# Kernel optimization log

Hardware: AMD Instinct MI355X
Metric: run time of the kernel (lower is better)

## Reference

```python
import jax, jax.numpy as jnp
import numpy as np

B, C, H, W = 32, 17, 256, 256


def setup_inputs() -> dict:
    key = jax.random.key(0)
    k1, k2 = jax.random.split(key)
    inp = jax.random.normal(k1, (B, C, H, W), dtype=jnp.float32)
    tgt = jax.random.normal(k2, (B, C, H, W), dtype=jnp.float32)
    masks = jnp.zeros((B, C, H, W), dtype=bool)  # unused by forward
    hull = jnp.zeros((B, 1, H, W), dtype=bool)   # unused by forward
    return {"input": inp, "target": tgt, "masks": masks, "hull": hull}


def reference(input, target, masks, hull):
    # m1: per-(batch, channel) mask of positive target pixels
    m1 = target > 0.0                                  # [B,C,H,W] bool
    # m2: per-batch OR over channels, broadcast back to every channel.
    # (replaces the original O(B*C) Python double loop)
    m2 = jnp.any(m1, axis=1, keepdims=True)            # [B,1,H,W] bool
    diff = jnp.abs(input - target)                     # [B,C,H,W]
    f32 = jnp.float32
    # masked means without data-dependent shapes: sum(mask*diff)/sum(mask)
    mean1 = jnp.sum(jnp.where(m1, diff, f32(0))) / jnp.sum(m1).astype(f32)
    cnt2 = jnp.sum(m2).astype(f32) * f32(diff.shape[1])  # broadcast over C channels
    mean2 = jnp.sum(jnp.where(m2, diff, f32(0))) / cnt2
    return (mean1 + mean2) / f32(2)
```

## Files before the change

kernel.cpp:

```cpp
#include <hip/hip_runtime.h>


#define QPB      16384
#define N_CH     17
#define N_BATCH  32
#define N_QUADS  (N_BATCH * QPB)
#define N_BLOCKS 2048

struct Slot {
    float s1;
    float s2;
    unsigned int c1;
    unsigned int c2;
};

__global__ __launch_bounds__(256) void heatloss_stage1(
    const float* __restrict__ inp, const float* __restrict__ tgt,
    Slot* __restrict__ slots) {

    const int blk = (blockIdx.x & 7) * (N_BLOCKS / 8) + (blockIdx.x >> 3);
    const int q = blk * 256 + threadIdx.x;
    const int b = q >> 14;
    const int r = q & (QPB - 1);

    const float4* __restrict__ tp = (const float4*)tgt + (size_t)b * (N_CH * QPB) + r;
    const float4* __restrict__ xp = (const float4*)inp + (size_t)b * (N_CH * QPB) + r;

    float4 tb[N_CH], xb[N_CH];
    #pragma unroll
    for (int c = 0; c < N_CH; ++c) tb[c] = tp[(size_t)c * QPB];
    #pragma unroll
    for (int c = 0; c < N_CH; ++c) xb[c] = xp[(size_t)c * QPB];

    __builtin_amdgcn_sched_barrier(0);

    float s1 = 0.0f;
    unsigned int c1 = 0u;
    float sa0 = 0.f, sa1 = 0.f, sa2 = 0.f, sa3 = 0.f;
    bool a0 = false, a1 = false, a2 = false, a3 = false;

    #pragma unroll
    for (int c = 0; c < N_CH; ++c) {
        float4 t = tb[c];
        float4 x = xb[c];
        float d0 = fabsf(x.x - t.x);
        float d1 = fabsf(x.y - t.y);
        float d2 = fabsf(x.z - t.z);
        float d3 = fabsf(x.w - t.w);
        bool p0 = t.x > 0.f, p1 = t.y > 0.f, p2 = t.z > 0.f, p3 = t.w > 0.f;
        sa0 += d0; sa1 += d1; sa2 += d2; sa3 += d3;
        s1 += p0 ? d0 : 0.f;  c1 += p0 ? 1u : 0u;  a0 = a0 || p0;
        s1 += p1 ? d1 : 0.f;  c1 += p1 ? 1u : 0u;  a1 = a1 || p1;
        s1 += p2 ? d2 : 0.f;  c1 += p2 ? 1u : 0u;  a2 = a2 || p2;
        s1 += p3 ? d3 : 0.f;  c1 += p3 ? 1u : 0u;  a3 = a3 || p3;
    }
    float s2 = (a0 ? sa0 : 0.f) + (a1 ? sa1 : 0.f) + (a2 ? sa2 : 0.f) + (a3 ? sa3 : 0.f);
    unsigned int c2 = (a0 ? 1u : 0u) + (a1 ? 1u : 0u) + (a2 ? 1u : 0u) + (a3 ? 1u : 0u);

    #pragma unroll
    for (int off = 32; off > 0; off >>= 1) {
        s1 += __shfl_down(s1, off);
        s2 += __shfl_down(s2, off);
        c1 += __shfl_down(c1, off);
        c2 += __shfl_down(c2, off);
    }

    __shared__ float ls1[4], ls2[4];
    __shared__ unsigned int lc1[4], lc2[4];
    const int wave = threadIdx.x >> 6;
    const int lane = threadIdx.x & 63;
    if (lane == 0) {
        ls1[wave] = s1; ls2[wave] = s2;
        lc1[wave] = c1; lc2[wave] = c2;
    }
    __syncthreads();
    if (threadIdx.x == 0) {
        Slot sl;
        sl.s1 = ls1[0] + ls1[1] + ls1[2] + ls1[3];
        sl.s2 = ls2[0] + ls2[1] + ls2[2] + ls2[3];
        sl.c1 = lc1[0] + lc1[1] + lc1[2] + lc1[3];
        sl.c2 = lc2[0] + lc2[1] + lc2[2] + lc2[3];
        slots[blockIdx.x] = sl;
    }
}

__global__ __launch_bounds__(256) void heatloss_stage2(
    const Slot* __restrict__ slots, float* __restrict__ out) {

    float s1 = 0.f, s2 = 0.f;
    unsigned int c1 = 0u, c2 = 0u;
    for (int i = threadIdx.x; i < N_BLOCKS; i += 256) {
        Slot sl = slots[i];
        s1 += sl.s1; s2 += sl.s2; c1 += sl.c1; c2 += sl.c2;
    }
    #pragma unroll
    for (int off = 32; off > 0; off >>= 1) {
        s1 += __shfl_down(s1, off);
        s2 += __shfl_down(s2, off);
        c1 += __shfl_down(c1, off);
        c2 += __shfl_down(c2, off);
    }
    __shared__ float ls1[4], ls2[4];
    __shared__ unsigned int lc1[4], lc2[4];
    const int wave = threadIdx.x >> 6;
    const int lane = threadIdx.x & 63;
    if (lane == 0) {
        ls1[wave] = s1; ls2[wave] = s2;
        lc1[wave] = c1; lc2[wave] = c2;
    }
    __syncthreads();
    if (threadIdx.x == 0) {
        float S1 = ls1[0] + ls1[1] + ls1[2] + ls1[3];
        float S2 = ls2[0] + ls2[1] + ls2[2] + ls2[3];
        float C1 = (float)(lc1[0] + lc1[1] + lc1[2] + lc1[3]);
        float C2 = (float)(lc2[0] + lc2[1] + lc2[2] + lc2[3]);
        float mean1 = S1 / C1;
        float mean2 = S2 / (C2 * (float)N_CH);
        out[0] = 0.5f * (mean1 + mean2);
    }
}

extern "C" void kernel_launch(void* const* d_in, const int* in_sizes, int n_in,
                              void* d_out, int out_size, void* d_ws, size_t ws_size,
                              hipStream_t stream) {
    const float* inp = (const float*)d_in[0];
    const float* tgt = (const float*)d_in[1];
    float* out = (float*)d_out;
    Slot* slots = (Slot*)d_ws;

    heatloss_stage1<<<N_BLOCKS, 256, 0, stream>>>(inp, tgt, slots);
    heatloss_stage2<<<1, 256, 0, stream>>>(slots, out);
}
```

Before: 346.8 us.

## Process four quads per thread with nontemporal loads and fewer blocks

Each thread now handles four pixel quads, so the grid shrinks fourfold to 512 blocks. Global loads use nontemporal hints and are interleaved with the compute inside the channel loop instead of being batched up front behind a sched_barrier. The aim is to cut cache pollution and per-block overhead on a pure streaming reduction. In exchange, 512 blocks may underfill the GPU's CUs and leave less memory parallelism to hide DRAM latency.

Measured after the change: 339.5 us, median of 2. 2.1% less time.

```diff
diff --git a/kernel.cpp b/kernel.cpp
--- a/kernel.cpp
+++ b/kernel.cpp
@@ -4,8 +4,13 @@
 #define QPB      16384
 #define N_CH     17
 #define N_BATCH  32
-#define N_QUADS  (N_BATCH * QPB)
-#define N_BLOCKS 2048
+#define THREADS  256
+#define G        4
+#define QUADS_PER_BLOCK (THREADS * G)
+#define BLK_PER_BATCH   (QPB / QUADS_PER_BLOCK)
+#define N_BLOCKS (N_BATCH * BLK_PER_BATCH)
+
+typedef float f32x4 __attribute__((ext_vector_type(4)));
 
 struct Slot {
     float s1;
@@ -14,48 +19,61 @@
     unsigned int c2;
 };
 
+__device__ __forceinline__ f32x4 ntload(const f32x4* p) {
+    return __builtin_nontemporal_load(p);
+}
+
 __global__ __launch_bounds__(256) void heatloss_stage1(
     const float* __restrict__ inp, const float* __restrict__ tgt,
     Slot* __restrict__ slots) {
 
     const int blk = (blockIdx.x & 7) * (N_BLOCKS / 8) + (blockIdx.x >> 3);
-    const int q = blk * 256 + threadIdx.x;
-    const int b = q >> 14;
-    const int r = q & (QPB - 1);
+    const int b  = blk >> 4;
+    const int rb = (blk & (BLK_PER_BATCH - 1)) * QUADS_PER_BLOCK;
 
-    const float4* __restrict__ tp = (const float4*)tgt + (size_t)b * (N_CH * QPB) + r;
-    const float4* __restrict__ xp = (const float4*)inp + (size_t)b * (N_CH * QPB) + r;
-
-    float4 tb[N_CH], xb[N_CH];
-    #pragma unroll
-    for (int c = 0; c < N_CH; ++c) tb[c] = tp[(size_t)c * QPB];
-    #pragma unroll
-    for (int c = 0; c < N_CH; ++c) xb[c] = xp[(size_t)c * QPB];
-
-    __builtin_amdgcn_sched_barrier(0);
+    const size_t base = (size_t)b * (N_CH * QPB) + rb + threadIdx.x;
+    const f32x4* __restrict__ tp = (const f32x4*)tgt + base;
+    const f32x4* __restrict__ xp = (const f32x4*)inp + base;
 
     float s1 = 0.0f;
     unsigned int c1 = 0u;
-    float sa0 = 0.f, sa1 = 0.f, sa2 = 0.f, sa3 = 0.f;
-    bool a0 = false, a1 = false, a2 = false, a3 = false;
+    float sa[G][4];
+    bool  an[G][4];
+    #pragma unroll
+    for (int g = 0; g < G; ++g)
+        #pragma unroll
+        for (int j = 0; j < 4; ++j) { sa[g][j] = 0.f; an[g][j] = false; }
 
     #pragma unroll
     for (int c = 0; c < N_CH; ++c) {
-        float4 t = tb[c];
-        float4 x = xb[c];
-        float d0 = fabsf(x.x - t.x);
-        float d1 = fabsf(x.y - t.y);
-        float d2 = fabsf(x.z - t.z);
-        float d3 = fabsf(x.w - t.w);
-        bool p0 = t.x > 0.f, p1 = t.y > 0.f, p2 = t.z > 0.f, p3 = t.w > 0.f;
-        sa0 += d0; sa1 += d1; sa2 += d2; sa3 += d3;
-        s1 += p0 ? d0 : 0.f;  c1 += p0 ? 1u : 0u;  a0 = a0 || p0;
-        s1 += p1 ? d1 : 0.f;  c1 += p1 ? 1u : 0u;  a1 = a1 || p1;
-        s1 += p2 ? d2 : 0.f;  c1 += p2 ? 1u : 0u;  a2 = a2 || p2;
-        s1 += p3 ? d3 : 0.f;  c1 += p3 ? 1u : 0u;  a3 = a3 || p3;
+        #pragma unroll
+        for (int g = 0; g < G; ++g) {
+            const size_t off = (size_t)c * QPB + (size_t)g * THREADS;
+            f32x4 t = ntload(tp + off);
+            f32x4 x = ntload(xp + off);
+            float d0 = fabsf(x.x - t.x);
+            float d1 = fabsf(x.y - t.y);
+            float d2 = fabsf(x.z - t.z);
+            float d3 = fabsf(x.w - t.w);
+            bool p0 = t.x > 0.f, p1 = t.y > 0.f, p2 = t.z > 0.f, p3 = t.w > 0.f;
+            sa[g][0] += d0; sa[g][1] += d1; sa[g][2] += d2; sa[g][3] += d3;
+            s1 += p0 ? d0 : 0.f;  c1 += p0 ? 1u : 0u;  an[g][0] = an[g][0] || p0;
+            s1 += p1 ? d1 : 0.f;  c1 += p1 ? 1u : 0u;  an[g][1] = an[g][1] || p1;
+            s1 += p2 ? d2 : 0.f;  c1 += p2 ? 1u : 0u;  an[g][2] = an[g][2] || p2;
+            s1 += p3 ? d3 : 0.f;  c1 += p3 ? 1u : 0u;  an[g][3] = an[g][3] || p3;
+        }
     }
-    float s2 = (a0 ? sa0 : 0.f) + (a1 ? sa1 : 0.f) + (a2 ? sa2 : 0.f) + (a3 ? sa3 : 0.f);
-    unsigned int c2 = (a0 ? 1u : 0u) + (a1 ? 1u : 0u) + (a2 ? 1u : 0u) + (a3 ? 1u : 0u);
+
+    float s2 = 0.f;
+    unsigned int c2 = 0u;
+    #pragma unroll
+    for (int g = 0; g < G; ++g) {
+        #pragma unroll
+        for (int j = 0; j < 4; ++j) {
+            s2 += an[g][j] ? sa[g][j] : 0.f;
+            c2 += an[g][j] ? 1u : 0u;
+        }
+    }
 
     #pragma unroll
     for (int off = 32; off > 0; off >>= 1) {
@@ -128,6 +146,6 @@
     float* out = (float*)d_out;
     Slot* slots = (Slot*)d_ws;
 
-    heatloss_stage1<<<N_BLOCKS, 256, 0, stream>>>(inp, tgt, slots);
+    heatloss_stage1<<<N_BLOCKS, THREADS, 0, stream>>>(inp, tgt, slots);
     heatloss_stage2<<<1, 256, 0, stream>>>(slots, out);
 }
```
